# Performance work log

Hardware: AMD Instinct MI355X
Metric: run time of the kernel (lower is better)

Reference implementation:

```python
import jax, jax.numpy as jnp
import numpy as np

N, D, P_CB, L_MAX = 32768, 512, 256, 8  # rows, embed dim, codebook size, log2(num_vectors)
LAMBDA_C, LAMBDA_P = 0.1, 0.33


def setup_inputs() -> dict:
    key = jax.random.key(0)
    k1, k2, k3, k4 = jax.random.split(key, 4)
    inputs = jax.random.normal(k1, (N, D), jnp.float32)
    # torch: codebook.weight.data.uniform_(-1/p, 1/p)
    codebook = jax.random.uniform(k2, (P_CB, D), jnp.float32, -1.0 / P_CB, 1.0 / P_CB)
    prev_vecs = jax.random.normal(k3, (P_CB, D), jnp.float32)
    # one uniform draw per codeword per active-level (replaces random.random() loop)
    noise_u = jax.random.uniform(k4, (L_MAX, P_CB), jnp.float32)
    correct_p = jnp.array([0.9], jnp.float32)
    return {"inputs": inputs, "codebook": codebook, "prev_vecs": prev_vecs,
            "correct_p": correct_p, "noise_u": noise_u, "num_vectors": 256}


def _mse(a, b):
    return jnp.mean((a - b) ** 2)


def _quantize_level(flat, codebook, cp, u, n_act):
    """cdist -> argmin -> noisy-channel column remap -> codeword gather."""
    actives = codebook[:n_act]                                # [n_act, D]
    # squared euclidean distances [N, n_act]
    dist = (jnp.sum(flat ** 2, axis=1, keepdims=True)
            + jnp.sum(actives ** 2, axis=1)
            - 2.0 * flat @ actives.T)
    idx = jnp.argmin(dist, axis=1)                            # [N]
    p_cb = codebook.shape[0]
    ar = jnp.arange(p_cb)
    # torch loop: if u<=cp keep column i, else copy column (i+1+integer)%p
    integer = jnp.floor((u - cp) / ((1.0 - cp) / p_cb)).astype(jnp.int32)
    src = jnp.where(u <= cp, ar, (ar + 1 + integer) % p_cb)   # [p_cb]
    # transmitted[n, i] = onehot(idx)[n, src[i]]; quantized = transmitted @ codebook
    # => quantized[n] = sum_{i: src[i]==idx[n]} codebook[i] = T[idx[n]]
    T = jax.ops.segment_sum(codebook, src, num_segments=p_cb)  # [p_cb, D]
    return T[idx]                                             # [N, D]


def reference(inputs, codebook, prev_vecs, correct_p, noise_u, num_vectors):
    cp = correct_p[0]
    L = int(np.log2(num_vectors))
    flat = inputs.reshape(-1, codebook.shape[1])
    sg = jax.lax.stop_gradient

    quants = [_quantize_level(flat, codebook, cp, noise_u[l], 2 ** (l + 1)).reshape(inputs.shape)
              for l in range(L)]
    actives = codebook[:num_vectors]  # final-iteration actives slice (as in torch)

    outs, losses = [], []
    for l in range(L):
        q_latent = _mse(quants[l], sg(inputs))
        if l == 0:
            e_latent, prox = _mse(sg(quants[l]), inputs), 0.0
        elif l == 1:
            e_latent = _mse(sg(quants[l]), inputs)
            prox = 1 * LAMBDA_P * _mse(prev_vecs[:2], actives[:2])
        else:
            e_latent = 0.0
            prox = LAMBDA_P * _mse(prev_vecs[:2 ** l], actives[:2 ** l])
        losses.append(q_latent + LAMBDA_C * e_latent + prox)
        # straight-through estimator
        outs.append(inputs + sg(quants[l] - inputs))
    return jnp.stack(outs), jnp.stack(losses), actives
```

## Files before the change

kernel.cpp:

```cpp
#include <hip/hip_runtime.h>
#include <math.h>

#define NN 32768
#define DD 512
#define PP 256
#define LV 8
#define GR 64
#define SSTR 257
#define EMIT_BLOCKS 4096

typedef float f4 __attribute__((ext_vector_type(4)));

__global__ __launch_bounds__(256) void prep_cnorm_kernel(const float* __restrict__ cb,
                                                         float* __restrict__ cnorm)
{
    __shared__ float xp[256];
    const int t = threadIdx.x;
    const int r = t & 63, q = t >> 6;
    const float* row = cb + (size_t)(blockIdx.x * 64 + r) * DD + q * 128;
    float s = 0.f;
    #pragma unroll 8
    for (int f = 0; f < 32; f++) {
        f4 v = *(const f4*)&row[f * 4];
        s += v.x * v.x; s += v.y * v.y; s += v.z * v.z; s += v.w * v.w;
    }
    xp[q * 64 + r] = s;
    __syncthreads();
    if (t < 64) cnorm[blockIdx.x * 64 + t] = (xp[t] + xp[64 + t]) + (xp[128 + t] + xp[192 + t]);
}

__global__ __launch_bounds__(256) void buildT_A_kernel(const float* __restrict__ cb,
                                                       const float* __restrict__ nu,
                                                       const float* __restrict__ cp_p,
                                                       float* __restrict__ T)
{
    const int l = blockIdx.x, p = blockIdx.y;
    const int t = threadIdx.x;
    const float cp = cp_p[0];
    #pragma unroll 1
    for (int it = 0; it < 8; it++) {
        int s = p * 16 + it * 2 + (t >> 7);
        float u = nu[l * PP + s];
        int d4 = (t & 127) * 4;
        f4 v = {0.f, 0.f, 0.f, 0.f};
        if (u <= cp) v = *(const f4*)&cb[(size_t)s * DD + d4];
        *(f4*)&T[((size_t)l * PP + s) * DD + d4] = v;
    }
}

__global__ __launch_bounds__(256) void buildT_B_kernel(const float* __restrict__ cb,
                                                       const float* __restrict__ nu,
                                                       const float* __restrict__ cp_p,
                                                       float* __restrict__ T)
{
    const int l = blockIdx.x;
    const int t = threadIdx.x;
    const float cp = cp_p[0];
    __shared__ int lj[PP], ls[PP];
    __shared__ int cnt;
    if (t == 0) cnt = 0;
    __syncthreads();
    float u = nu[l * PP + t];
    if (u > cp) {
        float step = (1.0f - cp) / 256.0f;
        int integer = (int)floorf((u - cp) / step);
        int src = (t + 1 + integer) & 255;
        int pos = atomicAdd(&cnt, 1);
        lj[pos] = t; ls[pos] = src;
    }
    __syncthreads();
    int n = cnt;
    for (int i = 0; i < n; i++) {
        int jj = lj[i], ss = ls[i];
        float*       dst = &T[((size_t)l * PP + ss) * DD];
        const float* sr  = &cb[(size_t)jj * DD];
        atomicAdd(&dst[t * 2],     sr[t * 2]);
        atomicAdd(&dst[t * 2 + 1], sr[t * 2 + 1]);
    }
}

__global__ __launch_bounds__(256, 4) void gemm_argmin_kernel(const float* __restrict__ x,
                                                             const float* __restrict__ cb,
                                                             const float* __restrict__ cnorm,
                                                             int* __restrict__ idx)
{
    __shared__ float sm[GR * SSTR];
    __shared__ float xn_sm[GR];
    __shared__ float xp[256];
    __shared__ float cnl[PP];

    const int t    = threadIdx.x;
    const int row0 = blockIdx.x * GR;
    const int cg   = t & 63;
    const int rg   = t >> 6;

    cnl[t] = cnorm[t];

    float acc[16][4];
    #pragma unroll
    for (int r = 0; r < 16; r++)
        #pragma unroll
        for (int c = 0; c < 4; c++) acc[r][c] = 0.f;

    for (int dc = 0; dc < DD; dc += 128) {
        __syncthreads();
        #pragma unroll
        for (int k = 0; k < 8; k++) {
            int i = t + k * 256;
            int r = i >> 5, f = i & 31;
            *(f4*)&sm[r * 128 + f * 4] = *(const f4*)&x[(size_t)(row0 + r) * DD + dc + f * 4];
        }
        __syncthreads();
        #pragma unroll 2
        for (int dd = 0; dd < 128; dd += 4) {
            f4 b0 = *(const f4*)&cb[(size_t)(cg      ) * DD + dc + dd];
            f4 b1 = *(const f4*)&cb[(size_t)(cg +  64) * DD + dc + dd];
            f4 b2 = *(const f4*)&cb[(size_t)(cg + 128) * DD + dc + dd];
            f4 b3 = *(const f4*)&cb[(size_t)(cg + 192) * DD + dc + dd];
            #pragma unroll
            for (int rr = 0; rr < 16; rr++) {
                f4 xa = *(const f4*)&sm[(rg * 16 + rr) * 128 + dd];
                acc[rr][0] += xa.x * b0.x; acc[rr][0] += xa.y * b0.y;
                acc[rr][0] += xa.z * b0.z; acc[rr][0] += xa.w * b0.w;
                acc[rr][1] += xa.x * b1.x; acc[rr][1] += xa.y * b1.y;
                acc[rr][1] += xa.z * b1.z; acc[rr][1] += xa.w * b1.w;
                acc[rr][2] += xa.x * b2.x; acc[rr][2] += xa.y * b2.y;
                acc[rr][2] += xa.z * b2.z; acc[rr][2] += xa.w * b2.w;
                acc[rr][3] += xa.x * b3.x; acc[rr][3] += xa.y * b3.y;
                acc[rr][3] += xa.z * b3.z; acc[rr][3] += xa.w * b3.w;
            }
        }
    }
    __syncthreads();

    #pragma unroll
    for (int rr = 0; rr < 16; rr++) {
        int r = rg * 16 + rr;
        sm[r * SSTR + cg      ] = -2.f * acc[rr][0];
        sm[r * SSTR + cg +  64] = -2.f * acc[rr][1];
        sm[r * SSTR + cg + 128] = -2.f * acc[rr][2];
        sm[r * SSTR + cg + 192] = -2.f * acc[rr][3];
    }

    {
        int r = t & 63, q = t >> 6;
        const float* xr = &x[(size_t)(row0 + r) * DD + q * 128];
        float s = 0.f;
        #pragma unroll 8
        for (int f = 0; f < 32; f++) {
            f4 v = *(const f4*)&xr[f * 4];
            s += v.x * v.x; s += v.y * v.y; s += v.z * v.z; s += v.w * v.w;
        }
        xp[q * 64 + r] = s;
    }
    __syncthreads();
    if (t < 64) xn_sm[t] = (xp[t] + xp[64 + t]) + (xp[128 + t] + xp[192 + t]);
    __syncthreads();

    {
        int r = t & 63, lp = t >> 6;
        int n    = 4 << (2 * lp);
        int half = n >> 1;
        float xn = xn_sm[r];
        const float* sc = &sm[r * SSTR];
        float best = (xn + cnl[0]) + sc[0];
        int bi = 0;
        int* od = &idx[(size_t)(row0 + r) * LV + 2 * lp];
        for (int j = 1; j < n; j++) {
            float v = (xn + cnl[j]) + sc[j];
            if (v < best) { best = v; bi = j; }
            if (j + 1 == half) od[0] = bi;
        }
        od[1] = bi;
    }
}

__global__ __launch_bounds__(256) void emit_kernel(const float* __restrict__ x,
                                                   const float* __restrict__ T,
                                                   const int* __restrict__ idx,
                                                   float* __restrict__ out,
                                                   float* __restrict__ partial)
{
    __shared__ int   idx_sm[64];
    __shared__ float red[4 * LV];
    const int t    = threadIdx.x;
    const int row0 = blockIdx.x * 8;
    if (t < 64) idx_sm[t] = idx[(size_t)row0 * LV + t];
    __syncthreads();

    float sse[LV];
    #pragma unroll
    for (int l = 0; l < LV; l++) sse[l] = 0.f;

    #pragma unroll 1
    for (int it = 0; it < 4; it++) {
        int rl = it * 2 + (t >> 7);
        int r  = row0 + rl;
        int d4 = (t & 127) * 4;
        f4 xv = __builtin_nontemporal_load((const f4*)&x[(size_t)r * DD + d4]);
        #pragma unroll
        for (int l = 0; l < LV; l++) {
            int id = idx_sm[rl * LV + l];
            f4 q = *(const f4*)&T[((size_t)l * PP + id) * DD + d4];
            float dx0 = q.x - xv.x, dx1 = q.y - xv.y, dx2 = q.z - xv.z, dx3 = q.w - xv.w;
            f4 o;
            o.x = xv.x + dx0; o.y = xv.y + dx1; o.z = xv.z + dx2; o.w = xv.w + dx3;
            __builtin_nontemporal_store(o, (f4*)&out[((size_t)l * NN + r) * DD + d4]);
            sse[l] += dx0 * dx0; sse[l] += dx1 * dx1; sse[l] += dx2 * dx2; sse[l] += dx3 * dx3;
        }
    }
    #pragma unroll
    for (int l = 0; l < LV; l++) {
        float v = sse[l];
        #pragma unroll
        for (int off = 32; off; off >>= 1) v += __shfl_down(v, off);
        if ((t & 63) == 0) red[(t >> 6) * LV + l] = v;
    }
    __syncthreads();
    if (t < LV)
        partial[(size_t)t * EMIT_BLOCKS + blockIdx.x] =
            (red[t] + red[LV + t]) + (red[2 * LV + t] + red[3 * LV + t]);
}

__global__ __launch_bounds__(256) void actives_kernel(const float* __restrict__ cb,
                                                      const float* __restrict__ prev,
                                                      float* __restrict__ actv,
                                                      float* __restrict__ rowsse)
{
    const int t = threadIdx.x;
    size_t i = (size_t)blockIdx.x * 2048 + (size_t)t * 8;
    int row = (int)(i >> 9);
    f4 c0 = *(const f4*)&cb[i];
    f4 c1 = *(const f4*)&cb[i + 4];
    *(f4*)&actv[i]     = c0;
    *(f4*)&actv[i + 4] = c1;
    f4 p0 = *(const f4*)&prev[i];
    f4 p1 = *(const f4*)&prev[i + 4];
    float s = 0.f;
    s += (p0.x - c0.x) * (p0.x - c0.x); s += (p0.y - c0.y) * (p0.y - c0.y);
    s += (p0.z - c0.z) * (p0.z - c0.z); s += (p0.w - c0.w) * (p0.w - c0.w);
    s += (p1.x - c1.x) * (p1.x - c1.x); s += (p1.y - c1.y) * (p1.y - c1.y);
    s += (p1.z - c1.z) * (p1.z - c1.z); s += (p1.w - c1.w) * (p1.w - c1.w);
    #pragma unroll
    for (int off = 32; off; off >>= 1) s += __shfl_down(s, off);
    if ((t & 63) == 0) rowsse[row] = s;
}

__global__ __launch_bounds__(256) void finalize_kernel(const float* __restrict__ partial,
                                                       const float* __restrict__ rowsse,
                                                       float* __restrict__ losses)
{
    __shared__ float ssev[LV];
    __shared__ float rs[PP];
    const int t = threadIdx.x;
    const int l = t >> 5, i = t & 31;
    float s = 0.f;
    for (int k = 0; k < EMIT_BLOCKS / 32; k++)
        s += partial[(size_t)l * EMIT_BLOCKS + i + k * 32];
    #pragma unroll
    for (int off = 16; off; off >>= 1) s += __shfl_down(s, off, 32);
    if (i == 0) ssev[l] = s;
    rs[t] = rowsse[t];
    __syncthreads();
    if (t == 0) {
        const float inv_nd = 1.0f / ((float)NN * (float)DD);
        float pacc = 0.f;
        int j = 0;
        for (int l2 = 0; l2 < LV; l2++) {
            float q = ssev[l2] * inv_nd;
            float e = (l2 <= 1) ? q : 0.f;
            float prox = 0.f;
            if (l2 >= 1) {
                int np_ = 1 << l2;
                while (j < np_) { pacc += rs[j]; j++; }
                prox = 0.33f * (pacc / ((float)np_ * (float)DD));
            }
            losses[l2] = q + 0.1f * e + prox;
        }
    }
}

extern "C" void kernel_launch(void* const* d_in, const int* in_sizes, int n_in,
                              void* d_out, int out_size, void* d_ws, size_t ws_size,
                              hipStream_t stream)
{
    const float* x    = (const float*)d_in[0];
    const float* cb   = (const float*)d_in[1];
    const float* prev = (const float*)d_in[2];
    const float* cp   = (const float*)d_in[3];
    const float* nu   = (const float*)d_in[4];

    float* T       = (float*)d_ws;
    float* cnorm   = T + (size_t)LV * PP * DD;
    float* partial = cnorm + PP;
    float* rowsse  = partial + LV * EMIT_BLOCKS;
    int*   idx     = (int*)(rowsse + PP);

    float* out    = (float*)d_out;
    float* losses = out + (size_t)LV * NN * DD;
    float* actv   = losses + LV;

    prep_cnorm_kernel<<<4, 256, 0, stream>>>(cb, cnorm);
    buildT_A_kernel<<<dim3(LV, 16), 256, 0, stream>>>(cb, nu, cp, T);
    buildT_B_kernel<<<LV, 256, 0, stream>>>(cb, nu, cp, T);
    gemm_argmin_kernel<<<NN / GR, 256, 0, stream>>>(x, cb, cnorm, idx);
    emit_kernel<<<EMIT_BLOCKS, 256, 0, stream>>>(x, T, idx, out, partial);
    actives_kernel<<<64, 256, 0, stream>>>(cb, prev, actv, rowsse);
    finalize_kernel<<<1, 256, 0, stream>>>(partial, rowsse, losses);
}
```

Before: 762.7 us.

## Transpose codebook and replace shared-memory argmin with in-register shuffle reduction

Adds a transposed codebook (cbT) built in the prep kernel. This lets the GEMM read contiguous 8-column vectors per thread, with each thread owning 8 rows by 8 codewords instead of 16 rows by 4 strided codewords. The argmin no longer writes distances to shared memory and scans serially. It packs each distance and its index into a 64-bit key and reduces with min and wave shuffles, which yields the prefix-level argmins for every level in one pass. The kernel's launch-bounds occupancy hint drops from 4 to 2 blocks and shared memory shrinks. The total runtime is dominated by the emit kernel's output writes, so the end-to-end effect may be limited.

Result: no change. 763.7 us (+0.1%).

```diff
diff --git a/kernel.cpp b/kernel.cpp
--- a/kernel.cpp
+++ b/kernel.cpp
@@ -6,27 +6,46 @@
 #define PP 256
 #define LV 8
 #define GR 64
-#define SSTR 257
 #define EMIT_BLOCKS 4096
 
 typedef float f4 __attribute__((ext_vector_type(4)));
 
-__global__ __launch_bounds__(256) void prep_cnorm_kernel(const float* __restrict__ cb,
-                                                         float* __restrict__ cnorm)
-{
-    __shared__ float xp[256];
-    const int t = threadIdx.x;
-    const int r = t & 63, q = t >> 6;
-    const float* row = cb + (size_t)(blockIdx.x * 64 + r) * DD + q * 128;
-    float s = 0.f;
-    #pragma unroll 8
-    for (int f = 0; f < 32; f++) {
-        f4 v = *(const f4*)&row[f * 4];
-        s += v.x * v.x; s += v.y * v.y; s += v.z * v.z; s += v.w * v.w;
-    }
-    xp[q * 64 + r] = s;
-    __syncthreads();
-    if (t < 64) cnorm[blockIdx.x * 64 + t] = (xp[t] + xp[64 + t]) + (xp[128 + t] + xp[192 + t]);
+__device__ __forceinline__ unsigned long long umin64(unsigned long long a, unsigned long long b)
+{
+    return b < a ? b : a;
+}
+
+__global__ __launch_bounds__(256) void prep_kernel(const float* __restrict__ cb,
+                                                   float* __restrict__ cnorm,
+                                                   float* __restrict__ cbT)
+{
+    const int t = threadIdx.x;
+    if (blockIdx.x < 4) {
+        __shared__ float xp[256];
+        const int r = t & 63, q = t >> 6;
+        const float* row = cb + (size_t)(blockIdx.x * 64 + r) * DD + q * 128;
+        float s = 0.f;
+        #pragma unroll 8
+        for (int f = 0; f < 32; f++) {
+            f4 v = *(const f4*)&row[f * 4];
+            s += v.x * v.x; s += v.y * v.y; s += v.z * v.z; s += v.w * v.w;
+        }
+        xp[q * 64 + r] = s;
+        __syncthreads();
+        if (t < 64) cnorm[blockIdx.x * 64 + t] = (xp[t] + xp[64 + t]) + (xp[128 + t] + xp[192 + t]);
+    } else {
+        const int d0 = (blockIdx.x - 4) * 8;
+        f4 v0 = *(const f4*)&cb[(size_t)t * DD + d0];
+        f4 v1 = *(const f4*)&cb[(size_t)t * DD + d0 + 4];
+        cbT[(size_t)(d0 + 0) * PP + t] = v0.x;
+        cbT[(size_t)(d0 + 1) * PP + t] = v0.y;
+        cbT[(size_t)(d0 + 2) * PP + t] = v0.z;
+        cbT[(size_t)(d0 + 3) * PP + t] = v0.w;
+        cbT[(size_t)(d0 + 4) * PP + t] = v1.x;
+        cbT[(size_t)(d0 + 5) * PP + t] = v1.y;
+        cbT[(size_t)(d0 + 6) * PP + t] = v1.z;
+        cbT[(size_t)(d0 + 7) * PP + t] = v1.w;
+    }
 }
 
 __global__ __launch_bounds__(256) void buildT_A_kernel(const float* __restrict__ cb,
@@ -79,28 +98,31 @@
     }
 }
 
-__global__ __launch_bounds__(256, 4) void gemm_argmin_kernel(const float* __restrict__ x,
-                                                             const float* __restrict__ cb,
+__global__ __launch_bounds__(256, 2) void gemm_argmin_kernel(const float* __restrict__ x,
+                                                             const float* __restrict__ cbT,
                                                              const float* __restrict__ cnorm,
                                                              int* __restrict__ idx)
 {
-    __shared__ float sm[GR * SSTR];
+    __shared__ float sm[GR * 128];
+    __shared__ float xp[256];
     __shared__ float xn_sm[GR];
-    __shared__ float xp[256];
-    __shared__ float cnl[PP];
-
-    const int t    = threadIdx.x;
-    const int row0 = blockIdx.x * GR;
-    const int cg   = t & 63;
-    const int rg   = t >> 6;
-
-    cnl[t] = cnorm[t];
-
-    float acc[16][4];
-    #pragma unroll
-    for (int r = 0; r < 16; r++)
+
+    const int t       = threadIdx.x;
+    const int row0    = blockIdx.x * GR;
+    const int cl      = t & 31;
+    const int c0      = cl * 8;
+    const int rowbase = (t >> 6) * 16 + ((t >> 5) & 1) * 8;
+    const float* xrow = sm + rowbase * 128;
+
+    f4 cn0 = *(const f4*)&cnorm[c0];
+    f4 cn1 = *(const f4*)&cnorm[c0 + 4];
+
+    f4 acc0[8], acc1[8];
+    {
+        f4 z = {0.f, 0.f, 0.f, 0.f};
         #pragma unroll
-        for (int c = 0; c < 4; c++) acc[r][c] = 0.f;
+        for (int r = 0; r < 8; r++) { acc0[r] = z; acc1[r] = z; }
+    }
 
     for (int dc = 0; dc < DD; dc += 128) {
         __syncthreads();
@@ -111,39 +133,38 @@
             *(f4*)&sm[r * 128 + f * 4] = *(const f4*)&x[(size_t)(row0 + r) * DD + dc + f * 4];
         }
         __syncthreads();
-        #pragma unroll 2
+        const float* bbase = cbT + (size_t)dc * PP + c0;
+        #pragma unroll 1
         for (int dd = 0; dd < 128; dd += 4) {
-            f4 b0 = *(const f4*)&cb[(size_t)(cg      ) * DD + dc + dd];
-            f4 b1 = *(const f4*)&cb[(size_t)(cg +  64) * DD + dc + dd];
-            f4 b2 = *(const f4*)&cb[(size_t)(cg + 128) * DD + dc + dd];
-            f4 b3 = *(const f4*)&cb[(size_t)(cg + 192) * DD + dc + dd];
+            const float* bp = bbase + (size_t)dd * PP;
+            f4 b00 = *(const f4*)&bp[0];
+            f4 b01 = *(const f4*)&bp[4];
+            f4 b10 = *(const f4*)&bp[PP];
+            f4 b11 = *(const f4*)&bp[PP + 4];
+            f4 b20 = *(const f4*)&bp[2 * PP];
+            f4 b21 = *(const f4*)&bp[2 * PP + 4];
+            f4 b30 = *(const f4*)&bp[3 * PP];
+            f4 b31 = *(const f4*)&bp[3 * PP + 4];
+            f4 xa[8];
             #pragma unroll
-            for (int rr = 0; rr < 16; rr++) {
-                f4 xa = *(const f4*)&sm[(rg * 16 + rr) * 128 + dd];
-                acc[rr][0] += xa.x * b0.x; acc[rr][0] += xa.y * b0.y;
-                acc[rr][0] += xa.z * b0.z; acc[rr][0] += xa.w * b0.w;
-                acc[rr][1] += xa.x * b1.x; acc[rr][1] += xa.y * b1.y;
-                acc[rr][1] += xa.z * b1.z; acc[rr][1] += xa.w * b1.w;
-                acc[rr][2] += xa.x * b2.x; acc[rr][2] += xa.y * b2.y;
-                acc[rr][2] += xa.z * b2.z; acc[rr][2] += xa.w * b2.w;
-                acc[rr][3] += xa.x * b3.x; acc[rr][3] += xa.y * b3.y;
-                acc[rr][3] += xa.z * b3.z; acc[rr][3] += xa.w * b3.w;
+            for (int rr = 0; rr < 8; rr++) xa[rr] = *(const f4*)&xrow[rr * 128 + dd];
+            #pragma unroll
+            for (int rr = 0; rr < 8; rr++) {
+                acc0[rr] += xa[rr].x * b00;
+                acc0[rr] += xa[rr].y * b10;
+                acc0[rr] += xa[rr].z * b20;
+                acc0[rr] += xa[rr].w * b30;
+                acc1[rr] += xa[rr].x * b01;
+                acc1[rr] += xa[rr].y * b11;
+                acc1[rr] += xa[rr].z * b21;
+                acc1[rr] += xa[rr].w * b31;
             }
         }
     }
     __syncthreads();
 
-    #pragma unroll
-    for (int rr = 0; rr < 16; rr++) {
-        int r = rg * 16 + rr;
-        sm[r * SSTR + cg      ] = -2.f * acc[rr][0];
-        sm[r * SSTR + cg +  64] = -2.f * acc[rr][1];
-        sm[r * SSTR + cg + 128] = -2.f * acc[rr][2];
-        sm[r * SSTR + cg + 192] = -2.f * acc[rr][3];
-    }
-
     {
-        int r = t & 63, q = t >> 6;
+        const int r = t & 63, q = t >> 6;
         const float* xr = &x[(size_t)(row0 + r) * DD + q * 128];
         float s = 0.f;
         #pragma unroll 8
@@ -157,21 +178,45 @@
     if (t < 64) xn_sm[t] = (xp[t] + xp[64 + t]) + (xp[128 + t] + xp[192 + t]);
     __syncthreads();
 
-    {
-        int r = t & 63, lp = t >> 6;
-        int n    = 4 << (2 * lp);
-        int half = n >> 1;
-        float xn = xn_sm[r];
-        const float* sc = &sm[r * SSTR];
-        float best = (xn + cnl[0]) + sc[0];
-        int bi = 0;
-        int* od = &idx[(size_t)(row0 + r) * LV + 2 * lp];
-        for (int j = 1; j < n; j++) {
-            float v = (xn + cnl[j]) + sc[j];
-            if (v < best) { best = v; bi = j; }
-            if (j + 1 == half) od[0] = bi;
-        }
-        od[1] = bi;
+    #pragma unroll 1
+    for (int rr = 0; rr < 8; rr++) {
+        const float xn = xn_sm[rowbase + rr];
+        float a0 = (xn + cn0.x) + (-2.f * acc0[rr].x);
+        float a1 = (xn + cn0.y) + (-2.f * acc0[rr].y);
+        float a2 = (xn + cn0.z) + (-2.f * acc0[rr].z);
+        float a3 = (xn + cn0.w) + (-2.f * acc0[rr].w);
+        float a4 = (xn + cn1.x) + (-2.f * acc1[rr].x);
+        float a5 = (xn + cn1.y) + (-2.f * acc1[rr].y);
+        float a6 = (xn + cn1.z) + (-2.f * acc1[rr].z);
+        float a7 = (xn + cn1.w) + (-2.f * acc1[rr].w);
+        unsigned long long k0 = ((unsigned long long)__float_as_uint(a0) << 32) | (unsigned)(c0 + 0);
+        unsigned long long k1 = ((unsigned long long)__float_as_uint(a1) << 32) | (unsigned)(c0 + 1);
+        unsigned long long k2 = ((unsigned long long)__float_as_uint(a2) << 32) | (unsigned)(c0 + 2);
+        unsigned long long k3 = ((unsigned long long)__float_as_uint(a3) << 32) | (unsigned)(c0 + 3);
+        unsigned long long k4 = ((unsigned long long)__float_as_uint(a4) << 32) | (unsigned)(c0 + 4);
+        unsigned long long k5 = ((unsigned long long)__float_as_uint(a5) << 32) | (unsigned)(c0 + 5);
+        unsigned long long k6 = ((unsigned long long)__float_as_uint(a6) << 32) | (unsigned)(c0 + 6);
+        unsigned long long k7 = ((unsigned long long)__float_as_uint(a7) << 32) | (unsigned)(c0 + 7);
+        unsigned long long s2 = umin64(k0, k1);
+        unsigned long long s4 = umin64(s2, umin64(k2, k3));
+        unsigned long long s8 = umin64(s4, umin64(umin64(k4, k5), umin64(k6, k7)));
+        unsigned long long m = s8, o;
+        o = __shfl_xor(m, 1);  m = umin64(m, o);  unsigned long long s16  = m;
+        o = __shfl_xor(m, 2);  m = umin64(m, o);  unsigned long long s32  = m;
+        o = __shfl_xor(m, 4);  m = umin64(m, o);  unsigned long long s64  = m;
+        o = __shfl_xor(m, 8);  m = umin64(m, o);  unsigned long long s128 = m;
+        o = __shfl_xor(m, 16); m = umin64(m, o);  unsigned long long s256 = m;
+        if (cl == 0) {
+            int* od = &idx[(size_t)(row0 + rowbase + rr) * LV];
+            od[0] = (int)(unsigned)s2;
+            od[1] = (int)(unsigned)s4;
+            od[2] = (int)(unsigned)s8;
+            od[3] = (int)(unsigned)s16;
+            od[4] = (int)(unsigned)s32;
+            od[5] = (int)(unsigned)s64;
+            od[6] = (int)(unsigned)s128;
+            od[7] = (int)(unsigned)s256;
+        }
     }
 }
 
@@ -294,16 +339,17 @@
     float* cnorm   = T + (size_t)LV * PP * DD;
     float* partial = cnorm + PP;
     float* rowsse  = partial + LV * EMIT_BLOCKS;
-    int*   idx     = (int*)(rowsse + PP);
+    float* cbT     = rowsse + PP;
+    int*   idx     = (int*)(cbT + (size_t)DD * PP);
 
     float* out    = (float*)d_out;
     float* losses = out + (size_t)LV * NN * DD;
     float* actv   = losses + LV;
 
-    prep_cnorm_kernel<<<4, 256, 0, stream>>>(cb, cnorm);
+    prep_kernel<<<68, 256, 0, stream>>>(cb, cnorm, cbT);
     buildT_A_kernel<<<dim3(LV, 16), 256, 0, stream>>>(cb, nu, cp, T);
     buildT_B_kernel<<<LV, 256, 0, stream>>>(cb, nu, cp, T);
-    gemm_argmin_kernel<<<NN / GR, 256, 0, stream>>>(x, cb, cnorm, idx);
+    gemm_argmin_kernel<<<NN / GR, 256, 0, stream>>>(x, cbT, cnorm, idx);
     emit_kernel<<<EMIT_BLOCKS, 256, 0, stream>>>(x, T, idx, out, partial);
     actives_kernel<<<64, 256, 0, stream>>>(cb, prev, actv, rowsse);
     finalize_kernel<<<1, 256, 0, stream>>>(partial, rowsse, losses);
```
